# Kernel tuning notes

Hardware: AMD Instinct MI355X
Metric: run time of the kernel (lower is better)

Reference implementation:

```python
import jax, jax.numpy as jnp
import numpy as np

BATCH = 65536
VEC = 512       # CLIP embedding dim
K = 1024        # num_cluster
GAMMA = 0.99
EPS = 1e-05


def setup_inputs() -> dict:
    key = jax.random.key(0)
    k1, k2, k3 = jax.random.split(key, 3)
    batch_vectors = jax.random.normal(k1, (BATCH, VEC), dtype=jnp.float32)
    weight = jax.random.normal(k2, (VEC, K), dtype=jnp.float32)        # codebook, stored (vec_size, num_cluster)
    cluster_size = jnp.ones((K,), dtype=jnp.float32)
    embed_avg = jax.random.normal(k3, (VEC, K), dtype=jnp.float32)
    return {
        "batch_vectors": batch_vectors,
        "weight": weight,
        "cluster_size": cluster_size,
        "embed_avg": embed_avg,
    }


def reference(batch_vectors, weight, cluster_size, embed_avg):
    """One minibatch_update step of clusteringEMA_torch.

    Returns the updated codebook `weight` of shape (vec_size, num_cluster).
    """
    gamma = GAMMA
    eps = EPS
    num_cluster = weight.shape[1]

    # nearest centroid: squared L2 distance has the same argmin as the L2 norm
    x2 = jnp.sum(batch_vectors * batch_vectors, axis=1, keepdims=True)   # (B,1)
    w2 = jnp.sum(weight * weight, axis=0)[None, :]                       # (1,K)
    dist2 = x2 + w2 - 2.0 * (batch_vectors @ weight)                     # (B,K)
    argmin = jnp.argmin(dist2, axis=-1)                                  # (B,)

    # per-cluster counts (one-hot sum), zeros replaced by 1
    counts = jnp.zeros((num_cluster,), dtype=batch_vectors.dtype).at[argmin].add(1.0)
    n_idx_choice = jnp.where(counts == 0, 1.0, counts)

    # EMA of cluster sizes
    new_cluster_size = gamma * cluster_size + (1.0 - gamma) * n_idx_choice

    # embed_sum = x^T @ onehot  == per-cluster sum of assigned vectors, (vec,K)
    embed_sum = jax.ops.segment_sum(batch_vectors, argmin, num_segments=num_cluster).T
    new_embed_avg = gamma * embed_avg + (1.0 - gamma) * embed_sum

    # Laplace-smoothed normalization
    n = jnp.sum(new_cluster_size)
    cs = (new_cluster_size + eps) / (n + num_cluster * eps) * n
    new_weight = new_embed_avg / cs[None, :]
    return new_weight
```

## Files before the change

### kernel.cpp

```cpp
#include <hip/hip_runtime.h>

typedef unsigned int uint;
typedef unsigned short ushort_t;
typedef unsigned long long u64;
typedef __attribute__((ext_vector_type(4))) float f32x4;
typedef __attribute__((ext_vector_type(8))) __bf16 bf16x8;
typedef __attribute__((ext_vector_type(8))) unsigned short us8;

#define BATCH 65536
#define VEC 512
#define K 1024
#define GAMMA 0.99f
#define EPS 1e-05f
#define SEG 64

#define BM 256
#define BN 256
#define NKT (VEC / 32)
#define BSLOT 2048

__device__ __forceinline__ ushort_t hi_of(float f) {
    return (ushort_t)(__float_as_uint(f) >> 16);
}
__device__ __forceinline__ ushort_t lo_of(float f) {
    float fhi = __uint_as_float(__float_as_uint(f) & 0xffff0000u);
    return (ushort_t)(__float_as_uint(f - fhi) >> 16);
}

__device__ __forceinline__ void gl16(const void* g, void* l) {
    __builtin_amdgcn_global_load_lds(
        (const __attribute__((address_space(1))) unsigned int*)g,
        (__attribute__((address_space(3))) unsigned int*)l, 16, 0, 0);
}

__device__ __forceinline__ void cvt8(f32x4 q0, f32x4 q1, bf16x8& h, bf16x8& l) {
    float ff[8] = {q0[0], q0[1], q0[2], q0[3], q1[0], q1[1], q1[2], q1[3]};
    us8 hh, ll;
#pragma unroll
    for (int j = 0; j < 8; ++j) {
        hh[j] = hi_of(ff[j]);
        ll[j] = lo_of(ff[j]);
    }
    h = __builtin_bit_cast(bf16x8, hh);
    l = __builtin_bit_cast(bf16x8, ll);
}

__global__ void k_pack_w(const float* __restrict__ w, us8* __restrict__ wpk,
                         float* __restrict__ w2p, u64* __restrict__ keys,
                         int* __restrict__ cc ) {
    __shared__ float lds[32][257];
    const int g = blockIdx.x;
    const int gx = g >> 4, ks = g & 15;
    const int t = threadIdx.x;

#pragma unroll
    for (int r = 0; r < 32; ++r)
        lds[r][t] = w[(size_t)(ks * 32 + r) * K + gx * 256 + t];
    __syncthreads();

    float s = 0.f;
#pragma unroll
    for (int r = 0; r < 32; ++r) { float f = lds[r][t]; s += f * f; }
    w2p[ks * K + gx * 256 + t] = s;

#pragma unroll
    for (int i = 0; i < 8; ++i) {
        const int o = i * 256 + t;
        const int lane = o & 63, half = (o >> 6) & 1, ct = o >> 7;
        const int cl = ct * 16 + (lane & 15);
        const int r0 = (lane >> 4) * 8;
        us8 v;
#pragma unroll
        for (int j = 0; j < 8; ++j) {
            float f = lds[r0 + j][cl];
            v[j] = half ? lo_of(f) : hi_of(f);
        }
        wpk[(size_t)g * BSLOT + o] = v;
    }

    u64* kp = keys + (size_t)g * 1024;
#pragma unroll
    for (int i = 0; i < 4; ++i) kp[i * 256 + t] = ~0ull;
    if (g < 8) cc[g * 256 + t] = 0;
}

__launch_bounds__(512, 2)
__global__ void k_gemm256(const float* __restrict__ x, const us8* __restrict__ wpk,
                          const float* __restrict__ w2p, u64* __restrict__ keys) {
    __shared__ us8 a_lds[2][2048];
    __shared__ us8 b_lds[2][2048];

    const int blk = blockIdx.x;
    const int gy = (blk & 7) * 32 + (blk >> 5);
    const int gx = (blk >> 3) & 3;
    const int t = threadIdx.x;
    const int lane = t & 63;
    const int wv = t >> 6;
    const int wm = wv >> 2;
    const int wn = wv & 3;

    const us8* bsrc = wpk + (size_t)gx * (NKT * BSLOT);

    const int slab0 = t >> 6;
    const int ls = t & 63;
    const float* xrow0 = x + (size_t)(gy * BM + slab0 * 16 + (ls & 15)) * VEC + (ls >> 4) * 8;
    const float* xrow1 = xrow0 + (size_t)128 * VEC;

    f32x4 av[4];
    auto aload = [&](int kt) {
        const float* p0 = xrow0 + kt * 32;
        av[0] = *(const f32x4*)(p0);
        av[1] = *(const f32x4*)(p0 + 4);
        const float* p1 = xrow1 + kt * 32;
        av[2] = *(const f32x4*)(p1);
        av[3] = *(const f32x4*)(p1 + 4);
    };
    auto awrite = [&](int buf) {
        bf16x8 h0, l0, h1, l1;
        cvt8(av[0], av[1], h0, l0);
        cvt8(av[2], av[3], h1, l1);
        const int o = slab0 * 128 + ls;
        a_lds[buf][o]          = __builtin_bit_cast(us8, h0);
        a_lds[buf][o + 64]     = __builtin_bit_cast(us8, l0);
        a_lds[buf][o + 1024]       = __builtin_bit_cast(us8, h1);
        a_lds[buf][o + 1024 + 64]  = __builtin_bit_cast(us8, l1);
    };
    auto bstage = [&](int buf, int kt) {
        const us8* sb = bsrc + (size_t)kt * BSLOT;
#pragma unroll
        for (int i = 0; i < 4; ++i)
            gl16(sb + i * 512 + t, &b_lds[buf][i * 512 + t]);
    };

    f32x4 acc[8][4];
#pragma unroll
    for (int i = 0; i < 8; ++i)
#pragma unroll
        for (int j = 0; j < 4; ++j) acc[i][j] = (f32x4){0.f, 0.f, 0.f, 0.f};

    aload(0);
    bstage(0, 0);
    awrite(0);
    __syncthreads();

    for (int tk = 0; tk < NKT; ++tk) {
        const int buf = tk & 1;
        const bool nx = (tk + 1 < NKT);
        if (nx) {
            aload(tk + 1);
            bstage(buf ^ 1, tk + 1);
        }

        const us8* A = &a_lds[buf][0];
        const us8* B = &b_lds[buf][0];

        bf16x8 bh[4], bl[4];
#pragma unroll
        for (int ct = 0; ct < 4; ++ct) {
            const int o = (wn * 4 + ct) * 128 + lane;
            bh[ct] = __builtin_bit_cast(bf16x8, B[o]);
            bl[ct] = __builtin_bit_cast(bf16x8, B[o + 64]);
        }
#pragma unroll
        for (int p = 0; p < 4; ++p) {
            bf16x8 ah[2], al[2];
#pragma unroll
            for (int i = 0; i < 2; ++i) {
                const int o = (wm * 8 + p * 2 + i) * 128 + lane;
                ah[i] = __builtin_bit_cast(bf16x8, A[o]);
                al[i] = __builtin_bit_cast(bf16x8, A[o + 64]);
            }
#pragma unroll
            for (int i = 0; i < 2; ++i)
#pragma unroll
                for (int ct = 0; ct < 4; ++ct) {
                    const int m = p * 2 + i;
                    acc[m][ct] = __builtin_amdgcn_mfma_f32_16x16x32_bf16(ah[i], bh[ct], acc[m][ct], 0, 0, 0);
                    acc[m][ct] = __builtin_amdgcn_mfma_f32_16x16x32_bf16(ah[i], bl[ct], acc[m][ct], 0, 0, 0);
                    acc[m][ct] = __builtin_amdgcn_mfma_f32_16x16x32_bf16(al[i], bh[ct], acc[m][ct], 0, 0, 0);
                }
        }
        if (nx) awrite(buf ^ 1);
        __syncthreads();
    }

    const int col_base = gx * BN + wn * 64;
    float w2c[4];
#pragma unroll
    for (int ct = 0; ct < 4; ++ct) {
        const int col = col_base + ct * 16 + (lane & 15);
        float s = 0.f;
#pragma unroll
        for (int p = 0; p < 16; ++p) s += w2p[p * K + col];
        w2c[ct] = s;
    }

#pragma unroll
    for (int rt = 0; rt < 8; ++rt) {
#pragma unroll
        for (int reg = 0; reg < 4; ++reg) {
            u64 km = ~0ull;
#pragma unroll
            for (int ct = 0; ct < 4; ++ct) {
                float dist = w2c[ct] - 2.0f * acc[rt][ct][reg];
                uint su = __float_as_uint(dist);
                su = (su & 0x80000000u) ? ~su : (su | 0x80000000u);
                const int col = col_base + ct * 16 + (lane & 15);
                u64 key = ((u64)su << 32) | (uint)col;
                km = key < km ? key : km;
            }
#pragma unroll
            for (int m = 1; m < 16; m <<= 1) {
                u64 o = __shfl_xor((unsigned long long)km, m);
                km = o < km ? o : km;
            }
            if ((lane & 15) == 0) {
                const int row = gy * BM + wm * 128 + rt * 16 + (lane >> 4) * 4 + reg;
                atomicMin((unsigned long long*)&keys[row], (unsigned long long)km);
            }
        }
    }
}

__global__ void k_hist(const u64* __restrict__ keys, int* __restrict__ counts,
                       float* __restrict__ esum) {
    const int b = blockIdx.x * blockDim.x + threadIdx.x;
    f32x4 z = {0.f, 0.f, 0.f, 0.f};
    ((f32x4*)esum)[b * 2]     = z;
    ((f32x4*)esum)[b * 2 + 1] = z;
    atomicAdd(&counts[(uint)(keys[b] & 0xffffffffull)], 1);
}

__global__ void k_scan(const int* __restrict__ counts,
                       const float* __restrict__ cluster_size,
                       int* __restrict__ offsets, float* __restrict__ cs) {
    __shared__ int wsum[16];
    __shared__ float fw[16];
    const int t = threadIdx.x;
    const int lane = t & 63, wid = t >> 6;
    const int c = counts[t];

    int s = c;
#pragma unroll
    for (int d = 1; d < 64; d <<= 1) {
        int o = __shfl_up(s, d);
        if (lane >= d) s += o;
    }
    float ncs = GAMMA * cluster_size[t] + (1.0f - GAMMA) * ((c == 0) ? 1.0f : (float)c);
    float fs = ncs;
#pragma unroll
    for (int d = 32; d > 0; d >>= 1) fs += __shfl_xor(fs, d);

    if (lane == 63) wsum[wid] = s;
    if (lane == 0) fw[wid] = fs;
    __syncthreads();
    if (wid == 0 && lane < 16) {
        int v = wsum[lane];
#pragma unroll
        for (int d = 1; d < 16; d <<= 1) {
            int o = __shfl_up(v, d);
            if (lane >= d) v += o;
        }
        wsum[lane] = v;
    }
    __syncthreads();
    const int base = wid ? wsum[wid - 1] : 0;
    offsets[t] = base + s - c;

    float n = 0.f;
#pragma unroll
    for (int i = 0; i < 16; ++i) n += fw[i];
    cs[t] = (ncs + EPS) / (n + (float)K * EPS) * n;
}

__global__ void k_scatter(const u64* __restrict__ keys, const int* __restrict__ offsets,
                          int* __restrict__ cursor, int* __restrict__ sorted,
                          int* __restrict__ sortedk) {
    const int b = blockIdx.x * blockDim.x + threadIdx.x;
    const int k = (int)(uint)(keys[b] & 0xffffffffull);
    const int pos = atomicAdd(&cursor[k], 1);
    sorted[offsets[k] + pos] = b;
    sortedk[offsets[k] + pos] = k;
}

__launch_bounds__(512)
__global__ void k_segred(const float* __restrict__ x, const int* __restrict__ sorted,
                         const int* __restrict__ sortedk, float* __restrict__ esum) {
    __shared__ int srow[SEG];
    __shared__ int skid[SEG];
    const int b = blockIdx.x;
    const int t = threadIdx.x;
    if (t < SEG) {
        srow[t] = sorted[b * SEG + t];
        skid[t] = sortedk[b * SEG + t];
    }
    __syncthreads();

    float a = 0.f;
    int cur = skid[0];
#pragma unroll 8
    for (int i = 0; i < SEG; ++i) {
        const int k = skid[i];
        if (k != cur) {
            atomicAdd(&esum[(size_t)cur * VEC + t], a);
            a = 0.f;
            cur = k;
        }
        a += x[(size_t)srow[i] * VEC + t];
    }
    atomicAdd(&esum[(size_t)cur * VEC + t], a);
}

__launch_bounds__(256)
__global__ void k_finalize(const float* __restrict__ esum, const float* __restrict__ embed_avg,
                           const float* __restrict__ cs, float* __restrict__ out) {
    __shared__ float tile[64][65];
    const int k0 = blockIdx.x * 64;
    const int v0 = blockIdx.y * 64;
    const int c = threadIdx.x & 63;
    const int r0 = threadIdx.x >> 6;
#pragma unroll
    for (int j = 0; j < 16; ++j) {
        const int r = r0 + j * 4;
        tile[r][c] = esum[(size_t)(k0 + r) * VEC + v0 + c];
    }
    __syncthreads();
    const float csk = cs[k0 + c];
#pragma unroll
    for (int j = 0; j < 16; ++j) {
        const int r = r0 + j * 4;
        const size_t o = (size_t)(v0 + r) * K + k0 + c;
        out[o] = (GAMMA * embed_avg[o] + (1.0f - GAMMA) * tile[c][r]) / csk;
    }
}

extern "C" void kernel_launch(void* const* d_in, const int* in_sizes, int n_in,
                              void* d_out, int out_size, void* d_ws, size_t ws_size,
                              hipStream_t stream) {
    const float* x            = (const float*)d_in[0];
    const float* w            = (const float*)d_in[1];
    const float* cluster_size = (const float*)d_in[2];
    const float* embed_avg    = (const float*)d_in[3];
    float* out = (float*)d_out;

    u64*   keys    = (u64*)d_ws;
    float* w2p     = (float*)(keys + BATCH);
    float* cs      = w2p + 16 * K;
    int*   counts  = (int*)(cs + K);
    int*   cursor  = counts + K;
    int*   offsets = cursor + K;
    int*   sorted  = offsets + K;
    int*   sortedk = sorted + BATCH;
    float* esum    = (float*)(sortedk + BATCH);
    us8*   wpk     = (us8*)(esum + (size_t)K * VEC);

    k_pack_w<<<64, 256, 0, stream>>>(w, wpk, w2p, keys, counts);
    k_gemm256<<<(BATCH / BM) * (K / BN), 512, 0, stream>>>(x, wpk, w2p, keys);
    k_hist<<<BATCH / 256, 256, 0, stream>>>(keys, counts, esum);
    k_scan<<<1, K, 0, stream>>>(counts, cluster_size, offsets, cs);
    k_scatter<<<BATCH / 256, 256, 0, stream>>>(keys, offsets, cursor, sorted, sortedk);
    k_segred<<<BATCH / SEG, 512, 0, stream>>>(x, sorted, sortedk, esum);
    k_finalize<<<dim3(K / 64, VEC / 64), 256, 0, stream>>>(esum, embed_avg, cs, out);
}
```

Measured before the change: 455.8 us.

## Replace split-bf16 GEMM with single bf16 pass plus top-2 margin recheck in fp32

Measured after the change: 388.0 us. 14.9% less time.

```diff
diff --git a/kernel.cpp b/kernel.cpp
--- a/kernel.cpp
+++ b/kernel.cpp
@@ -13,18 +13,13 @@
 #define GAMMA 0.99f
 #define EPS 1e-05f
 #define SEG 64
-
-#define BM 256
-#define BN 256
+#define MARGIN 0.75f
+
 #define NKT (VEC / 32)
-#define BSLOT 2048
-
-__device__ __forceinline__ ushort_t hi_of(float f) {
-    return (ushort_t)(__float_as_uint(f) >> 16);
-}
-__device__ __forceinline__ ushort_t lo_of(float f) {
-    float fhi = __uint_as_float(__float_as_uint(f) & 0xffff0000u);
-    return (ushort_t)(__float_as_uint(f - fhi) >> 16);
+
+__device__ __forceinline__ ushort_t rtn(float f) {
+    uint u = __float_as_uint(f);
+    return (ushort_t)((u + 0x7FFFu + ((u >> 16) & 1u)) >> 16);
 }
 
 __device__ __forceinline__ void gl16(const void* g, void* l) {
@@ -33,20 +28,13 @@
         (__attribute__((address_space(3))) unsigned int*)l, 16, 0, 0);
 }
 
-__device__ __forceinline__ void cvt8(f32x4 q0, f32x4 q1, bf16x8& h, bf16x8& l) {
-    float ff[8] = {q0[0], q0[1], q0[2], q0[3], q1[0], q1[1], q1[2], q1[3]};
-    us8 hh, ll;
-#pragma unroll
-    for (int j = 0; j < 8; ++j) {
-        hh[j] = hi_of(ff[j]);
-        ll[j] = lo_of(ff[j]);
-    }
-    h = __builtin_bit_cast(bf16x8, hh);
-    l = __builtin_bit_cast(bf16x8, ll);
+__device__ __forceinline__ float dec_key(uint e) {
+    uint b = (e & 0x80000000u) ? (e & 0x7FFFFFFFu) : ~e;
+    return __uint_as_float(b);
 }
 
 __global__ void k_pack_w(const float* __restrict__ w, us8* __restrict__ wpk,
-                         float* __restrict__ w2p, u64* __restrict__ keys,
+                         float* __restrict__ wT, float* __restrict__ w2p,
                          int* __restrict__ cc ) {
     __shared__ float lds[32][257];
     const int g = blockIdx.x;
@@ -64,34 +52,36 @@
     w2p[ks * K + gx * 256 + t] = s;
 
 #pragma unroll
-    for (int i = 0; i < 8; ++i) {
+    for (int i = 0; i < 4; ++i) {
         const int o = i * 256 + t;
-        const int lane = o & 63, half = (o >> 6) & 1, ct = o >> 7;
+        const int lane = o & 63, ct = o >> 6;
         const int cl = ct * 16 + (lane & 15);
         const int r0 = (lane >> 4) * 8;
         us8 v;
 #pragma unroll
-        for (int j = 0; j < 8; ++j) {
-            float f = lds[r0 + j][cl];
-            v[j] = half ? lo_of(f) : hi_of(f);
-        }
-        wpk[(size_t)g * BSLOT + o] = v;
-    }
-
-    u64* kp = keys + (size_t)g * 1024;
-#pragma unroll
-    for (int i = 0; i < 4; ++i) kp[i * 256 + t] = ~0ull;
+        for (int j = 0; j < 8; ++j) v[j] = rtn(lds[r0 + j][cl]);
+        wpk[(size_t)g * 1024 + o] = v;
+    }
+
+#pragma unroll
+    for (int rr = 0; rr < 8; ++rr) {
+        f32x4 v = {lds[rr * 4 + 0][t], lds[rr * 4 + 1][t], lds[rr * 4 + 2][t], lds[rr * 4 + 3][t]};
+        *(f32x4*)&wT[(size_t)(gx * 256 + t) * VEC + ks * 32 + rr * 4] = v;
+    }
+
     if (g < 8) cc[g * 256 + t] = 0;
-}
-
-__launch_bounds__(512, 2)
-__global__ void k_gemm256(const float* __restrict__ x, const us8* __restrict__ wpk,
-                          const float* __restrict__ w2p, u64* __restrict__ keys) {
-    __shared__ us8 a_lds[2][2048];
-    __shared__ us8 b_lds[2][2048];
+    if (g == 8 && t == 0) cc[2048] = 0;
+}
+
+__launch_bounds__(512, 4)
+__global__ void k_gemm(const float* __restrict__ x, const us8* __restrict__ wpk,
+                       const float* __restrict__ w2p,
+                       u64* __restrict__ keysA, u64* __restrict__ keysB) {
+    __shared__ us8 a_lds[2][512];
+    __shared__ us8 b_lds[2][1024];
 
     const int blk = blockIdx.x;
-    const int gy = (blk & 7) * 32 + (blk >> 5);
+    const int gy = (blk & 7) * 64 + ((blk >> 3) >> 2);
     const int gx = (blk >> 3) & 3;
     const int t = threadIdx.x;
     const int lane = t & 63;
@@ -99,42 +89,31 @@
     const int wm = wv >> 2;
     const int wn = wv & 3;
 
-    const us8* bsrc = wpk + (size_t)gx * (NKT * BSLOT);
-
-    const int slab0 = t >> 6;
-    const int ls = t & 63;
-    const float* xrow0 = x + (size_t)(gy * BM + slab0 * 16 + (ls & 15)) * VEC + (ls >> 4) * 8;
-    const float* xrow1 = xrow0 + (size_t)128 * VEC;
-
-    f32x4 av[4];
+    const us8* bsrc = wpk + (size_t)gx * (NKT * 1024);
+
+    const int al = t & 63;
+    const float* xp = x + (size_t)(gy * 128 + (t >> 6) * 16 + (al & 15)) * VEC + (al >> 4) * 8;
+    f32x4 av0, av1;
     auto aload = [&](int kt) {
-        const float* p0 = xrow0 + kt * 32;
-        av[0] = *(const f32x4*)(p0);
-        av[1] = *(const f32x4*)(p0 + 4);
-        const float* p1 = xrow1 + kt * 32;
-        av[2] = *(const f32x4*)(p1);
-        av[3] = *(const f32x4*)(p1 + 4);
+        const float* p = xp + kt * 32;
+        av0 = *(const f32x4*)p;
+        av1 = *(const f32x4*)(p + 4);
     };
     auto awrite = [&](int buf) {
-        bf16x8 h0, l0, h1, l1;
-        cvt8(av[0], av[1], h0, l0);
-        cvt8(av[2], av[3], h1, l1);
-        const int o = slab0 * 128 + ls;
-        a_lds[buf][o]          = __builtin_bit_cast(us8, h0);
-        a_lds[buf][o + 64]     = __builtin_bit_cast(us8, l0);
-        a_lds[buf][o + 1024]       = __builtin_bit_cast(us8, h1);
-        a_lds[buf][o + 1024 + 64]  = __builtin_bit_cast(us8, l1);
+        us8 h;
+#pragma unroll
+        for (int j = 0; j < 4; ++j) { h[j] = rtn(av0[j]); h[4 + j] = rtn(av1[j]); }
+        a_lds[buf][t] = h;
     };
     auto bstage = [&](int buf, int kt) {
-        const us8* sb = bsrc + (size_t)kt * BSLOT;
-#pragma unroll
-        for (int i = 0; i < 4; ++i)
-            gl16(sb + i * 512 + t, &b_lds[buf][i * 512 + t]);
+        const us8* sb = bsrc + (size_t)kt * 1024;
+        gl16(sb + t, &b_lds[buf][t]);
+        gl16(sb + 512 + t, &b_lds[buf][512 + t]);
     };
 
-    f32x4 acc[8][4];
-#pragma unroll
-    for (int i = 0; i < 8; ++i)
+    f32x4 acc[4][4];
+#pragma unroll
+    for (int i = 0; i < 4; ++i)
 #pragma unroll
         for (int j = 0; j < 4; ++j) acc[i][j] = (f32x4){0.f, 0.f, 0.f, 0.f};
 
@@ -150,41 +129,22 @@
             aload(tk + 1);
             bstage(buf ^ 1, tk + 1);
         }
-
-        const us8* A = &a_lds[buf][0];
-        const us8* B = &b_lds[buf][0];
-
-        bf16x8 bh[4], bl[4];
-#pragma unroll
-        for (int ct = 0; ct < 4; ++ct) {
-            const int o = (wn * 4 + ct) * 128 + lane;
-            bh[ct] = __builtin_bit_cast(bf16x8, B[o]);
-            bl[ct] = __builtin_bit_cast(bf16x8, B[o + 64]);
-        }
-#pragma unroll
-        for (int p = 0; p < 4; ++p) {
-            bf16x8 ah[2], al[2];
-#pragma unroll
-            for (int i = 0; i < 2; ++i) {
-                const int o = (wm * 8 + p * 2 + i) * 128 + lane;
-                ah[i] = __builtin_bit_cast(bf16x8, A[o]);
-                al[i] = __builtin_bit_cast(bf16x8, A[o + 64]);
-            }
-#pragma unroll
-            for (int i = 0; i < 2; ++i)
-#pragma unroll
-                for (int ct = 0; ct < 4; ++ct) {
-                    const int m = p * 2 + i;
-                    acc[m][ct] = __builtin_amdgcn_mfma_f32_16x16x32_bf16(ah[i], bh[ct], acc[m][ct], 0, 0, 0);
-                    acc[m][ct] = __builtin_amdgcn_mfma_f32_16x16x32_bf16(ah[i], bl[ct], acc[m][ct], 0, 0, 0);
-                    acc[m][ct] = __builtin_amdgcn_mfma_f32_16x16x32_bf16(al[i], bh[ct], acc[m][ct], 0, 0, 0);
-                }
+        bf16x8 bh[4];
+#pragma unroll
+        for (int ct = 0; ct < 4; ++ct)
+            bh[ct] = __builtin_bit_cast(bf16x8, b_lds[buf][(wn * 4 + ct) * 64 + lane]);
+#pragma unroll
+        for (int rt = 0; rt < 4; ++rt) {
+            bf16x8 ah = __builtin_bit_cast(bf16x8, a_lds[buf][(wm * 4 + rt) * 64 + lane]);
+#pragma unroll
+            for (int ct = 0; ct < 4; ++ct)
+                acc[rt][ct] = __builtin_amdgcn_mfma_f32_16x16x32_bf16(ah, bh[ct], acc[rt][ct], 0, 0, 0);
         }
         if (nx) awrite(buf ^ 1);
         __syncthreads();
     }
 
-    const int col_base = gx * BN + wn * 64;
+    const int col_base = gx * 256 + wn * 64;
     float w2c[4];
 #pragma unroll
     for (int ct = 0; ct < 4; ++ct) {
@@ -194,41 +154,112 @@
         for (int p = 0; p < 16; ++p) s += w2p[p * K + col];
         w2c[ct] = s;
     }
-
-#pragma unroll
-    for (int rt = 0; rt < 8; ++rt) {
+    const int slot = gx * 4 + wn;
+
+#pragma unroll
+    for (int rt = 0; rt < 4; ++rt) {
 #pragma unroll
         for (int reg = 0; reg < 4; ++reg) {
-            u64 km = ~0ull;
+            u64 k1 = ~0ull, k2 = ~0ull;
 #pragma unroll
             for (int ct = 0; ct < 4; ++ct) {
                 float dist = w2c[ct] - 2.0f * acc[rt][ct][reg];
                 uint su = __float_as_uint(dist);
                 su = (su & 0x80000000u) ? ~su : (su | 0x80000000u);
-                const int col = col_base + ct * 16 + (lane & 15);
-                u64 key = ((u64)su << 32) | (uint)col;
-                km = key < km ? key : km;
+                const u64 key = ((u64)su << 32) | (uint)(col_base + ct * 16 + (lane & 15));
+                if (key < k1) { k2 = k1; k1 = key; }
+                else if (key < k2) { k2 = key; }
             }
 #pragma unroll
             for (int m = 1; m < 16; m <<= 1) {
-                u64 o = __shfl_xor((unsigned long long)km, m);
-                km = o < km ? o : km;
+                u64 o1 = __shfl_xor((unsigned long long)k1, m);
+                u64 o2 = __shfl_xor((unsigned long long)k2, m);
+                u64 lo = k1 < o1 ? k1 : o1;
+                u64 hi = k1 < o1 ? o1 : k1;
+                u64 mn2 = k2 < o2 ? k2 : o2;
+                k1 = lo;
+                k2 = hi < mn2 ? hi : mn2;
             }
             if ((lane & 15) == 0) {
-                const int row = gy * BM + wm * 128 + rt * 16 + (lane >> 4) * 4 + reg;
-                atomicMin((unsigned long long*)&keys[row], (unsigned long long)km);
+                const int row = gy * 128 + wm * 64 + rt * 16 + (lane >> 4) * 4 + reg;
+                keysA[(size_t)slot * BATCH + row] = k1;
+                keysB[(size_t)slot * BATCH + row] = k2;
             }
         }
     }
 }
 
-__global__ void k_hist(const u64* __restrict__ keys, int* __restrict__ counts,
-                       float* __restrict__ esum) {
-    const int b = blockIdx.x * blockDim.x + threadIdx.x;
+__global__ void k_verify(const u64* __restrict__ keysA, const u64* __restrict__ keysB,
+                         int* __restrict__ am, int* __restrict__ counts,
+                         u64* __restrict__ list, int* __restrict__ listcnt,
+                         float* __restrict__ esum) {
+    const int r = blockIdx.x * 256 + threadIdx.x;
     f32x4 z = {0.f, 0.f, 0.f, 0.f};
-    ((f32x4*)esum)[b * 2]     = z;
-    ((f32x4*)esum)[b * 2 + 1] = z;
-    atomicAdd(&counts[(uint)(keys[b] & 0xffffffffull)], 1);
+    ((f32x4*)esum)[r * 2] = z;
+    ((f32x4*)esum)[r * 2 + 1] = z;
+
+    u64 m1 = ~0ull, s = ~0ull;
+    int i1 = 0;
+#pragma unroll
+    for (int i = 0; i < 16; ++i) {
+        u64 a = keysA[(size_t)i * BATCH + r];
+        if (a < m1) { s = m1; m1 = a; i1 = i; }
+        else if (a < s) s = a;
+    }
+    u64 b = keysB[(size_t)i1 * BATCH + r];
+    u64 m2 = s < b ? s : b;
+
+    const float d1 = dec_key((uint)(m1 >> 32));
+    const float d2 = dec_key((uint)(m2 >> 32));
+    const int c1 = (int)(uint)m1 & 1023;
+    const int c2 = (int)(uint)m2 & 1023;
+
+    if (d2 - d1 > MARGIN) {
+        am[r] = c1;
+        atomicAdd(&counts[c1], 1);
+    } else {
+        int p = atomicAdd(listcnt, 1);
+        list[p] = ((u64)(uint)r << 32) | ((uint)c1 << 10) | (uint)c2;
+    }
+}
+
+__launch_bounds__(256)
+__global__ void k_recheck(const float* __restrict__ x, const float* __restrict__ wT,
+                          const float* __restrict__ w2p, const u64* __restrict__ list,
+                          const int* __restrict__ listcnt, int* __restrict__ am,
+                          int* __restrict__ counts) {
+    const int gwid = (blockIdx.x * 256 + threadIdx.x) >> 6;
+    const int lane = threadIdx.x & 63;
+    const int n = *listcnt;
+    for (int idx = gwid; idx < n; idx += 1024) {
+        const u64 e = list[idx];
+        const int r = (int)(e >> 32);
+        const int c1 = (int)((e >> 10) & 1023);
+        const int c2 = (int)(e & 1023);
+        const f32x4 x0 = *(const f32x4*)&x[(size_t)r * VEC + lane * 8];
+        const f32x4 x1 = *(const f32x4*)&x[(size_t)r * VEC + lane * 8 + 4];
+        float d[2];
+        const int cc[2] = {c1, c2};
+#pragma unroll
+        for (int j = 0; j < 2; ++j) {
+            const int c = cc[j];
+            const f32x4 w0 = *(const f32x4*)&wT[(size_t)c * VEC + lane * 8];
+            const f32x4 w1 = *(const f32x4*)&wT[(size_t)c * VEC + lane * 8 + 4];
+            float p = x0[0] * w0[0] + x0[1] * w0[1] + x0[2] * w0[2] + x0[3] * w0[3]
+                    + x1[0] * w1[0] + x1[1] * w1[1] + x1[2] * w1[2] + x1[3] * w1[3];
+#pragma unroll
+            for (int m = 1; m < 64; m <<= 1) p += __shfl_xor(p, m);
+            float w2 = 0.f;
+#pragma unroll
+            for (int q = 0; q < 16; ++q) w2 += w2p[q * K + c];
+            d[j] = w2 - 2.0f * p;
+        }
+        const int win = (d[0] < d[1] || (d[0] == d[1] && c1 < c2)) ? c1 : c2;
+        if (lane == 0) {
+            am[r] = win;
+            atomicAdd(&counts[win], 1);
+        }
+    }
 }
 
 __global__ void k_scan(const int* __restrict__ counts,
@@ -273,11 +304,11 @@
     cs[t] = (ncs + EPS) / (n + (float)K * EPS) * n;
 }
 
-__global__ void k_scatter(const u64* __restrict__ keys, const int* __restrict__ offsets,
+__global__ void k_scatter(const int* __restrict__ am, const int* __restrict__ offsets,
                           int* __restrict__ cursor, int* __restrict__ sorted,
                           int* __restrict__ sortedk) {
     const int b = blockIdx.x * blockDim.x + threadIdx.x;
-    const int k = (int)(uint)(keys[b] & 0xffffffffull);
+    const int k = am[b];
     const int pos = atomicAdd(&cursor[k], 1);
     sorted[offsets[k] + pos] = b;
     sortedk[offsets[k] + pos] = k;
@@ -343,22 +374,29 @@
     const float* embed_avg    = (const float*)d_in[3];
     float* out = (float*)d_out;
 
-    u64*   keys    = (u64*)d_ws;
-    float* w2p     = (float*)(keys + BATCH);
+    u64*   keysA   = (u64*)d_ws;
+    u64*   keysB   = keysA + (size_t)16 * BATCH;
+    int*   am      = (int*)(keysB + (size_t)16 * BATCH);
+    u64*   list    = (u64*)(am + BATCH);
+    float* w2p     = (float*)(list + BATCH);
     float* cs      = w2p + 16 * K;
-    int*   counts  = (int*)(cs + K);
-    int*   cursor  = counts + K;
-    int*   offsets = cursor + K;
+    int*   cc      = (int*)(cs + K);
+    int*   counts  = cc;
+    int*   cursor  = cc + K;
+    int*   listcnt = cc + 2 * K;
+    int*   offsets = cc + 2 * K + 64;
     int*   sorted  = offsets + K;
     int*   sortedk = sorted + BATCH;
     float* esum    = (float*)(sortedk + BATCH);
     us8*   wpk     = (us8*)(esum + (size_t)K * VEC);
-
-    k_pack_w<<<64, 256, 0, stream>>>(w, wpk, w2p, keys, counts);
-    k_gemm256<<<(BATCH / BM) * (K / BN), 512, 0, stream>>>(x, wpk, w2p, keys);
-    k_hist<<<BATCH / 256, 256, 0, stream>>>(keys, counts, esum);
+    float* wT      = (float*)(wpk + (size_t)64 * 1024);
+
+    k_pack_w<<<64, 256, 0, stream>>>(w, wpk, wT, w2p, cc);
+    k_gemm<<<2048, 512, 0, stream>>>(x, wpk, w2p, keysA, keysB);
+    k_verify<<<BATCH / 256, 256, 0, stream>>>(keysA, keysB, am, counts, list, listcnt, esum);
+    k_recheck<<<256, 256, 0, stream>>>(x, wT, w2p, list, listcnt, am, counts);
     k_scan<<<1, K, 0, stream>>>(counts, cluster_size, offsets, cs);
-    k_scatter<<<BATCH / 256, 256, 0, stream>>>(keys, offsets, cursor, sorted, sortedk);
+    k_scatter<<<BATCH / 256, 256, 0, stream>>>(am, offsets, cursor, sorted, sortedk);
     k_segred<<<BATCH / SEG, 512, 0, stream>>>(x, sorted, sortedk, esum);
     k_finalize<<<dim3(K / 64, VEC / 64), 256, 0, stream>>>(esum, embed_avg, cs, out);
 }
```
